# Kernel tuning notes

Hardware: AMD Instinct MI355X
Metric: run time of the kernel (lower is better)

## Reference

```python
import jax, jax.numpy as jnp
import numpy as np

EPS = 1e-5
L1, L2 = 1e-3, 1e-3
HEADS, HEAD_DIM = 8, 16


def ln(x):
    # torch.nn.LayerNorm over last dim, affine params at init (gamma=1, beta=0)
    m = jnp.mean(x, axis=-1, keepdims=True)
    v = jnp.var(x, axis=-1, keepdims=True)
    return (x - m) / jnp.sqrt(v + EPS)


def setup_inputs() -> dict:
    key = jax.random.key(0)
    ks = jax.random.split(key, 10)
    B, N, Dn = 16, 1000, 64
    D = HEADS * HEAD_DIM  # 128
    return {
        "nodevec_fusion": jax.random.normal(ks[0], (B, N, Dn), jnp.float32),
        "nodevec_s": jax.random.normal(ks[1], (N, Dn), jnp.float32),
        "node_input": jax.random.normal(ks[2], (B, N, Dn), jnp.float32),
        "nodevec_dy": jax.random.normal(ks[3], (N, Dn), jnp.float32),
        "w_q": jax.random.normal(ks[4], (Dn, D), jnp.float32) * 0.1,
        "w_k": jax.random.normal(ks[5], (Dn, D), jnp.float32) * 0.1,
        "node_w": jax.random.normal(ks[6], (N, Dn), jnp.float32) * 0.1,
        "mlp_w": jax.random.normal(ks[7], (HEADS, HEADS), jnp.float32) * 0.1,
        "mlp_b": jnp.zeros((HEADS,), jnp.float32),
        "attn_linear": jax.random.normal(ks[8], (N, N), jnp.float32) * 0.03,
        "attn_linear_1": jax.random.normal(ks[9], (N, N), jnp.float32) * 0.03,
        "batch_size": 16,
    }


def reference(nodevec_fusion, nodevec_s, node_input, nodevec_dy,
              w_q, w_k, node_w, mlp_w, mlp_b, attn_linear, attn_linear_1,
              batch_size):
    B = batch_size
    N, Dn = nodevec_s.shape
    H, hd = HEADS, HEAD_DIM

    # static graph: softmax(relu(LN(S S^T)), axis=1)
    s = nodevec_s @ nodevec_s.T                     # [N,N]
    adj_static = jax.nn.softmax(jax.nn.relu(ln(s)), axis=1)

    fusion = ln(nodevec_fusion)                     # [B,N,Dn]
    static_graph_inf = ln(nodevec_dy @ nodevec_dy.T)  # [N,N]

    # einsum('bnd,nl->bnl'): d is summed out of x only
    nv11 = jnp.einsum('bnd,nl->bnl', fusion, node_w) + fusion  # [B,N,Dn]
    skip_atten = ln(jnp.einsum('bnd,bmd->bnm', nv11, nv11))    # [B,N,N]

    # query/key fc layers (leaky_relu(x @ W)), then split D -> (H, hd)
    q = jax.nn.leaky_relu(jnp.einsum('bnd,do->bno', fusion, w_q))  # [B,N,D]
    k = jax.nn.leaky_relu(jnp.einsum('bnd,do->bno', fusion, w_k))  # [B,N,D]
    q = q.transpose(0, 2, 1).reshape(B, H, hd, N).transpose(0, 1, 3, 2)  # [B,H,N,hd]
    k = k.transpose(0, 2, 1).reshape(B, H, hd, N)                        # [B,H,hd,N]

    attention = jnp.einsum('bhnd,bhdm->bhnm', q, k) / (hd ** 0.5)  # [B,H,N,N]
    # 1x1 conv mixing heads + residual (dropout = 0)
    attention = jnp.einsum('oh,bhnm->bonm', mlp_w, attention) \
        + mlp_b[None, :, None, None] + attention

    adj_bf = ln(jnp.sum(attention, axis=1)) + skip_atten           # [B,N,N]
    adj_af = jax.nn.relu(jnp.einsum('bnm,ml->bnl', ln(adj_bf), attn_linear))
    adj_af = jnp.einsum('bnm,ml->bnl', adj_af, attn_linear_1)
    dy_adj_inf = ln(adj_af + adj_bf)
    dy_adj = ln(dy_adj_inf + static_graph_inf[None])
    adj_dynamic = jax.nn.softmax(jax.nn.relu(dy_adj), axis=2)

    adj_static_b = jnp.broadcast_to(adj_static[None], (B, N, N))

    # graph loss: sum_ij ||x_i - x_j||^2 * A_ij via squared-distance matmul trick
    sq = jnp.sum(node_input * node_input, axis=-1)                 # [B,N]
    gram = jnp.einsum('bnd,bmd->bnm', node_input, node_input)      # [B,N,N]
    d2 = sq[:, :, None] + sq[:, None, :] - 2.0 * gram              # [B,N,N]
    dist_loss = jnp.sum(d2 * adj_static_b, axis=(1, 2))            # [B]
    f_norm = jnp.sum(adj_static_b * adj_static_b, axis=(1, 2))     # [B]
    gl_loss = dist_loss * L1 + f_norm * L2

    return adj_dynamic, adj_static_b, nodevec_s, gl_loss
```

## Files before the change

### kernel.cpp

```cpp
#include <hip/hip_runtime.h>

#define B_  16
#define N_  1000
#define NP  1024
#define DN  64
#define D_  128

typedef __attribute__((ext_vector_type(8))) short  short8;
typedef __attribute__((ext_vector_type(4))) float  f32x4;
typedef __attribute__((ext_vector_type(4))) unsigned short ushort4v;

__device__ __forceinline__ unsigned short f2bf(float v) {
  union { float f; unsigned int u; } c; c.f = v;
  unsigned int u = c.u;
  unsigned int r = (u + 0x7fffu + ((u >> 16) & 1u)) >> 16;
  return (unsigned short)r;
}
__device__ __forceinline__ float bf2f(unsigned short h) {
  union { unsigned int u; float f; } c; c.u = ((unsigned int)h) << 16; return c.f;
}

__device__ __forceinline__ void block_red2(float& a, float& b) {
  __shared__ float sb[8];
  __syncthreads();
  float ra = a, rb = b;
  #pragma unroll
  for (int o = 32; o > 0; o >>= 1) { ra += __shfl_down(ra, o); rb += __shfl_down(rb, o); }
  int w = threadIdx.x >> 6;
  if ((threadIdx.x & 63) == 0) { sb[w] = ra; sb[4 + w] = rb; }
  __syncthreads();
  a = sb[0] + sb[1] + sb[2] + sb[3];
  b = sb[4] + sb[5] + sb[6] + sb[7];
}

__device__ __forceinline__ void block_redmax(float& a) {
  __shared__ float sm[4];
  __syncthreads();
  float ra = a;
  #pragma unroll
  for (int o = 32; o > 0; o >>= 1) ra = fmaxf(ra, __shfl_down(ra, o));
  if ((threadIdx.x & 63) == 0) sm[threadIdx.x >> 6] = ra;
  __syncthreads();
  a = fmaxf(fmaxf(sm[0], sm[1]), fmaxf(sm[2], sm[3]));
}

__global__ void prep_kernel(const float* __restrict__ mlp_w, const float* __restrict__ mlp_b,
                            const float* __restrict__ w_q, const float* __restrict__ w_k,
                            float* __restrict__ weff, float* __restrict__ tr,
                            float* __restrict__ fnorm, float* __restrict__ colsum,
                            unsigned short* __restrict__ wt) {
  int t = threadIdx.x;
  if (t < 8) {
    float s = 1.f;
    for (int o = 0; o < 8; ++o) s += mlp_w[o * 8 + t];
    weff[t] = s;
  }
  if (t < 16) tr[t] = 0.f;
  if (t == 16) fnorm[0] = 0.f;
  colsum[t] = 0.f;
  for (int i = t; i < 256 * 64; i += 1024) {
    int col = i >> 6, d = i & 63;
    float v = (col < 128) ? w_q[d * D_ + col] : w_k[d * D_ + (col - 128)];
    wt[i] = f2bf(v);
  }
  (void)mlp_b;
}

__global__ void transpose_pad(const float* __restrict__ in, unsigned short* __restrict__ out) {
  __shared__ float tile[32][33];
  int bx = blockIdx.x * 32, by = blockIdx.y * 32;
  int tx = threadIdx.x, ty = threadIdx.y;
  #pragma unroll
  for (int i = 0; i < 32; i += 8) {
    int r = by + ty + i, c = bx + tx;
    tile[ty + i][tx] = (r < N_ && c < N_) ? in[(long)r * N_ + c] : 0.f;
  }
  __syncthreads();
  #pragma unroll
  for (int i = 0; i < 32; i += 8) {
    int r = bx + ty + i, c = by + tx;
    out[(long)r * NP + c] = f2bf(tile[tx][ty + i]);
  }
}

__global__ void gram_kernel(const float* __restrict__ X, float* __restrict__ C, int ldc) {
  __shared__ float Xi[16][65], Xj[16][65];
  int tx = threadIdx.x, ty = threadIdx.y;
  int i0 = blockIdx.y * 16, j0 = blockIdx.x * 16;
  #pragma unroll
  for (int kk = 0; kk < 64; kk += 16) {
    int r = i0 + ty;  Xi[ty][kk + tx] = (r < N_) ? X[(long)r * DN + kk + tx] : 0.f;
    int rj = j0 + ty; Xj[ty][kk + tx] = (rj < N_) ? X[(long)rj * DN + kk + tx] : 0.f;
  }
  __syncthreads();
  float acc = 0.f;
  #pragma unroll
  for (int d = 0; d < 64; ++d) acc += Xi[ty][d] * Xj[tx][d];
  int i = i0 + ty, j = j0 + tx;
  if (i < N_ && j < N_) C[(long)i * ldc + j] = acc;
}

__global__ void row_ln(float* __restrict__ base, int ld) {
  int tid = threadIdx.x;
  float* row = base + (long)blockIdx.x * ld;
  float x[4]; float s = 0.f, s2 = 0.f;
  #pragma unroll
  for (int i = 0; i < 4; ++i) {
    int idx = tid + i * 256;
    x[i] = (idx < N_) ? row[idx] : 0.f;
    s += x[i]; s2 += x[i] * x[i];
  }
  block_red2(s, s2);
  float mean = s * 1e-3f, var = s2 * 1e-3f - mean * mean;
  float r = rsqrtf(var + 1e-5f);
  #pragma unroll
  for (int i = 0; i < 4; ++i) {
    int idx = tid + i * 256;
    if (idx < N_) row[idx] = (x[i] - mean) * r;
  }
}

__global__ void row_ln_sm(float* __restrict__ mat, float* __restrict__ rowsum) {
  int n = blockIdx.x, tid = threadIdx.x;
  float* row = mat + (long)n * N_;
  float x[4]; float s = 0.f, s2 = 0.f;
  #pragma unroll
  for (int i = 0; i < 4; ++i) {
    int idx = tid + i * 256;
    x[i] = (idx < N_) ? row[idx] : 0.f;
    s += x[i]; s2 += x[i] * x[i];
  }
  block_red2(s, s2);
  float mean = s * 1e-3f, var = s2 * 1e-3f - mean * mean;
  float r = rsqrtf(var + 1e-5f);
  float mx = -1e30f;
  #pragma unroll
  for (int i = 0; i < 4; ++i) {
    int idx = tid + i * 256;
    if (idx < N_) { x[i] = fmaxf((x[i] - mean) * r, 0.f); mx = fmaxf(mx, x[i]); }
  }
  block_redmax(mx);
  float es = 0.f, d = 0.f;
  #pragma unroll
  for (int i = 0; i < 4; ++i) {
    int idx = tid + i * 256;
    if (idx < N_) { x[i] = __expf(x[i] - mx); es += x[i]; } else x[i] = 0.f;
  }
  block_red2(es, d);
  float inv = 1.f / es; float ps = 0.f;
  #pragma unroll
  for (int i = 0; i < 4; ++i) {
    int idx = tid + i * 256;
    if (idx < N_) { x[i] *= inv; row[idx] = x[i]; ps += x[i]; }
  }
  d = 0.f; block_red2(ps, d);
  if (tid == 0) rowsum[n] = ps;
}

__global__ __launch_bounds__(256)
void fusion_ln(const float* __restrict__ fus, const float* __restrict__ node_w,
               const float* __restrict__ node_input,
               unsigned short* __restrict__ fbf, unsigned short* __restrict__ nv11,
               float* __restrict__ sq) {
  int wid = blockIdx.x * 4 + (threadIdx.x >> 6);
  int lane = threadIdx.x & 63;
  #pragma unroll 1
  for (int r = 0; r < 16; ++r) {
    int row = wid * 16 + r;
    int b = row >> 10, n = row & 1023;
    long po = (long)row * DN + lane;
    if (n < N_) {
      long io = ((long)b * N_ + n) * DN + lane;
      float xv = fus[io];
      float s = xv, s2 = xv * xv;
      #pragma unroll
      for (int o = 32; o > 0; o >>= 1) { s += __shfl_xor(s, o); s2 += __shfl_xor(s2, o); }
      float mean = s * (1.f / DN);
      float var  = s2 * (1.f / DN) - mean * mean;
      float fv = (xv - mean) * rsqrtf(var + 1e-5f);
      float rs = fv;
      #pragma unroll
      for (int o = 32; o > 0; o >>= 1) rs += __shfl_xor(rs, o);
      fbf[po]  = f2bf(fv);
      nv11[po] = f2bf(rs * node_w[(long)n * DN + lane] + fv);
      float xi = node_input[io];
      float q2 = xi * xi;
      #pragma unroll
      for (int o = 32; o > 0; o >>= 1) q2 += __shfl_xor(q2, o);
      if (lane == 0) sq[(long)b * N_ + n] = q2;
    } else {
      fbf[po] = 0; nv11[po] = 0;
    }
  }
}

#define GLOAD_LDS16(gp, lp) \
  __builtin_amdgcn_global_load_lds((const __attribute__((address_space(1))) void*)(gp), \
                                   (__attribute__((address_space(3))) void*)(lp), 16, 0, 0)

template<int EPI>
__global__ __launch_bounds__(256, 2)
void gemm_bt(const unsigned short* __restrict__ X, long xbs, int ldx,
             const unsigned short* __restrict__ Y, long ybs, int ldy,
             int K,
             unsigned short* __restrict__ outB, long obsB,
             const float* __restrict__ weff) {
  __shared__ __align__(16) short As[128 * 32];
  __shared__ __align__(16) short Bs[128 * 32];
  const int tid = threadIdx.x;
  const int b  = blockIdx.z;
  const int m0 = blockIdx.x * 128;
  const int n0 = blockIdx.y * 128;
  const unsigned short* Xb = X + (long)b * xbs + (long)m0 * ldx;
  const unsigned short* Yb = Y + (long)b * ybs + (long)n0 * ldy;

  const int lane = tid & 63, w = tid >> 6;
  const int wm = (w >> 1) * 64, wn = (w & 1) * 64;
  const int fr = lane & 15, kg = lane >> 4;

  const int sr = tid >> 2;
  const int ks = tid & 3;
  const int c1 = ((ks ^ ((sr >> 1) & 3)) * 8);
  const int c2 = ((ks ^ (((sr + 64) >> 1) & 3)) * 8);

  f32x4 acc[4][4];
  #pragma unroll
  for (int mi = 0; mi < 4; ++mi)
    #pragma unroll
    for (int ni = 0; ni < 4; ++ni)
      acc[mi][ni] = (f32x4){0.f, 0.f, 0.f, 0.f};

  const short* Asp = (const short*)As;
  const short* Bsp = (const short*)Bs;

  for (int k0 = 0; k0 < K; k0 += 32) {
    GLOAD_LDS16(Xb + (long)sr * ldx + k0 + c1,        (char*)As + tid * 16);
    GLOAD_LDS16(Xb + (long)(sr + 64) * ldx + k0 + c2, (char*)As + 4096 + tid * 16);
    GLOAD_LDS16(Yb + (long)sr * ldy + k0 + c1,        (char*)Bs + tid * 16);
    GLOAD_LDS16(Yb + (long)(sr + 64) * ldy + k0 + c2, (char*)Bs + 4096 + tid * 16);
    __syncthreads();
    short8 av[4], bv[4];
    #pragma unroll
    for (int mi = 0; mi < 4; ++mi) {
      int r = wm + mi * 16 + fr;
      av[mi] = *(const short8*)&Asp[r * 32 + ((kg ^ ((r >> 1) & 3)) * 8)];
    }
    #pragma unroll
    for (int ni = 0; ni < 4; ++ni) {
      int r = wn + ni * 16 + fr;
      bv[ni] = *(const short8*)&Bsp[r * 32 + ((kg ^ ((r >> 1) & 3)) * 8)];
    }
    #pragma unroll
    for (int mi = 0; mi < 4; ++mi)
      #pragma unroll
      for (int ni = 0; ni < 4; ++ni)
        acc[mi][ni] = __builtin_amdgcn_mfma_f32_16x16x32_bf16(av[mi], bv[ni], acc[mi][ni], 0, 0, 0);
    __syncthreads();
  }

  if (EPI == 1) {
    unsigned short* ob = outB + (long)b * obsB;
    #pragma unroll
    for (int mi = 0; mi < 4; ++mi) {
      #pragma unroll
      for (int ni = 0; ni < 4; ++ni) {
        int col  = n0 + wn + ni * 16 + fr;
        int rowb = m0 + wm + mi * 16 + kg * 4;
        #pragma unroll
        for (int j = 0; j < 4; ++j)
          ob[(long)(rowb + j) * NP + col] = f2bf(fmaxf(acc[mi][ni][j], 0.f));
      }
    }
  } else if (EPI == 2) {
    unsigned short* ob = outB;
    #pragma unroll
    for (int mi = 0; mi < 4; ++mi) {
      #pragma unroll
      for (int ni = 0; ni < 4; ++ni) {
        int col  = n0 + wn + ni * 16 + fr;
        int rowb = m0 + wm + mi * 16 + kg * 4;
        float sc = (col < 128) ? weff[col >> 4] * 0.25f : 1.f;
        #pragma unroll
        for (int j = 0; j < 4; ++j) {
          float v = acc[mi][ni][j];
          v = (v > 0.f) ? v : 0.01f * v;
          ob[(long)(rowb + j) * 256 + col] = f2bf(v * sc);
        }
      }
    }
  } else {
    unsigned short* ob = outB + (long)b * obsB;
    #pragma unroll
    for (int mi = 0; mi < 4; ++mi) {
      #pragma unroll
      for (int ni = 0; ni < 4; ++ni) {
        int col  = n0 + wn + ni * 16 + fr;
        int rowb = m0 + wm + mi * 16 + kg * 4;
        #pragma unroll
        for (int j = 0; j < 4; ++j)
          ob[(long)(rowb + j) * NP + col] = f2bf(acc[mi][ni][j]);
      }
    }
  }
}

__global__ __launch_bounds__(256)
void row_combine1(const unsigned short* __restrict__ apre, const unsigned short* __restrict__ skip,
                  unsigned short* __restrict__ adjbf, unsigned short* __restrict__ tbf) {
  int n = blockIdx.x, b = blockIdx.y, tid = threadIdx.x;
  long ro = ((long)b * NP + n) * NP + tid * 4;
  ushort4v a4 = *(const ushort4v*)(apre + ro);
  ushort4v s4 = *(const ushort4v*)(skip + ro);
  float xa[4], xs[4];
  float sa = 0.f, sa2 = 0.f, ss = 0.f, ss2 = 0.f;
  #pragma unroll
  for (int j = 0; j < 4; ++j) {
    bool mm = (tid * 4 + j) < N_;
    xa[j] = mm ? bf2f(a4[j]) : 0.f;
    xs[j] = mm ? bf2f(s4[j]) : 0.f;
    sa += xa[j]; sa2 += xa[j] * xa[j];
    ss += xs[j]; ss2 += xs[j] * xs[j];
  }
  block_red2(sa, sa2);
  block_red2(ss, ss2);
  float ma = sa * 1e-3f, ra = rsqrtf(sa2 * 1e-3f - ma * ma + 1e-5f);
  float ms = ss * 1e-3f, rs = rsqrtf(ss2 * 1e-3f - ms * ms + 1e-5f);
  float y[4]; float sy = 0.f, sy2 = 0.f;
  #pragma unroll
  for (int j = 0; j < 4; ++j) {
    y[j] = ((tid * 4 + j) < N_) ? (xa[j] - ma) * ra + (xs[j] - ms) * rs : 0.f;
    sy += y[j]; sy2 += y[j] * y[j];
  }
  block_red2(sy, sy2);
  float my = sy * 1e-3f, ry = rsqrtf(sy2 * 1e-3f - my * my + 1e-5f);
  ushort4v o1, o2;
  #pragma unroll
  for (int j = 0; j < 4; ++j) {
    o1[j] = f2bf(y[j]);
    o2[j] = ((tid * 4 + j) < N_) ? f2bf((y[j] - my) * ry) : (unsigned short)0;
  }
  *(ushort4v*)(adjbf + ro) = o1;
  *(ushort4v*)(tbf + ro) = o2;
}

__global__ __launch_bounds__(256)
void row_final(const unsigned short* __restrict__ g2, const unsigned short* __restrict__ adjbf,
               const float* __restrict__ sgi, float* __restrict__ outp) {
  int n = blockIdx.x, b = blockIdx.y, tid = threadIdx.x;
  long ro = ((long)b * NP + n) * NP + tid * 4;
  ushort4v g4 = *(const ushort4v*)(g2 + ro);
  ushort4v a4 = *(const ushort4v*)(adjbf + ro);
  float4 gr = *(const float4*)(sgi + (long)n * NP + tid * 4);
  const float* grp = (const float*)&gr;
  float x[4]; float s = 0.f, s2 = 0.f;
  #pragma unroll
  for (int j = 0; j < 4; ++j) {
    x[j] = ((tid * 4 + j) < N_) ? bf2f(g4[j]) + bf2f(a4[j]) : 0.f;
    s += x[j]; s2 += x[j] * x[j];
  }
  block_red2(s, s2);
  float m1 = s * 1e-3f, r1 = rsqrtf(s2 * 1e-3f - m1 * m1 + 1e-5f);
  s = 0.f; s2 = 0.f;
  #pragma unroll
  for (int j = 0; j < 4; ++j) {
    x[j] = ((tid * 4 + j) < N_) ? (x[j] - m1) * r1 + grp[j] : 0.f;
    s += x[j]; s2 += x[j] * x[j];
  }
  block_red2(s, s2);
  float m2 = s * 1e-3f, r2 = rsqrtf(s2 * 1e-3f - m2 * m2 + 1e-5f);
  float mx = -1e30f;
  #pragma unroll
  for (int j = 0; j < 4; ++j) {
    if ((tid * 4 + j) < N_) { x[j] = fmaxf((x[j] - m2) * r2, 0.f); mx = fmaxf(mx, x[j]); }
  }
  block_redmax(mx);
  float es = 0.f, dd = 0.f;
  #pragma unroll
  for (int j = 0; j < 4; ++j) {
    if ((tid * 4 + j) < N_) { x[j] = __expf(x[j] - mx); es += x[j]; } else x[j] = 0.f;
  }
  block_red2(es, dd);
  float inv = 1.f / es;
  if (tid < 250) {
    float4 o = make_float4(x[0] * inv, x[1] * inv, x[2] * inv, x[3] * inv);
    *(float4*)(outp + (long)b * 1000000 + (long)n * N_ + tid * 4) = o;
  }
}

__global__ void broadcast_static(const float* __restrict__ adjs, float* __restrict__ out1) {
  long i = (long)blockIdx.x * 256 + threadIdx.x;
  if (i < 250000) {
    float4 v = ((const float4*)adjs)[i];
    #pragma unroll
    for (int b = 0; b < B_; ++b) ((float4*)out1)[(long)b * 250000 + i] = v;
  }
}

__global__ void copy_s(const float* __restrict__ src, float* __restrict__ dst) {
  int i = blockIdx.x * 256 + threadIdx.x;
  if (i < N_ * DN) dst[i] = src[i];
}

__global__ void colsum_fnorm(const float* __restrict__ adjs, float* __restrict__ colsum,
                             float* __restrict__ fnorm) {
  int m = blockIdx.x * 256 + threadIdx.x;
  int n0 = blockIdx.y * 63;
  int ne = min(n0 + 63, N_);
  float c = 0.f, f = 0.f;
  if (m < N_) {
    for (int n = n0; n < ne; ++n) { float v = adjs[(long)n * N_ + m]; c += v; f += v * v; }
    atomicAdd(&colsum[m], c);
  }
  float d = 0.f; block_red2(f, d);
  if (threadIdx.x == 0) atomicAdd(fnorm, f);
}

__global__ __launch_bounds__(256)
void trace_kernel(const float* __restrict__ adjs, const float* __restrict__ x,
                  float* __restrict__ tr) {
  __shared__ float A_s[64 * 64];
  __shared__ float X_s[64 * 64];
  const int tid = threadIdx.x;
  const int tx = tid & 15, ty = tid >> 4;
  const int m0 = blockIdx.x * 64;
  const int b  = blockIdx.y;
  const int nseg = blockIdx.z;
  const float* xb = x + (long)b * (N_ * DN);

  float acc[4][4];
  #pragma unroll
  for (int i = 0; i < 4; ++i)
    #pragma unroll
    for (int j = 0; j < 4; ++j) acc[i][j] = 0.f;

  for (int cc = 0; cc < 4; ++cc) {
    int n0 = (nseg * 4 + cc) * 64;
    #pragma unroll
    for (int k = 0; k < 16; ++k) {
      int i = tid + k * 256;
      int nn = i >> 6, cm = i & 63;
      int n = n0 + nn;
      A_s[i] = (n < N_ && (m0 + cm) < N_) ? adjs[(long)n * N_ + m0 + cm] : 0.f;
      X_s[i] = (n < N_) ? xb[(long)n * DN + cm] : 0.f;
    }
    __syncthreads();
    #pragma unroll 8
    for (int nn = 0; nn < 64; ++nn) {
      float4 av = *(const float4*)&A_s[nn * 64 + ty * 4];
      float4 xv = *(const float4*)&X_s[nn * 64 + tx * 4];
      #pragma unroll
      for (int i = 0; i < 4; ++i) {
        float a = (&av.x)[i];
        acc[i][0] += a * xv.x;
        acc[i][1] += a * xv.y;
        acc[i][2] += a * xv.z;
        acc[i][3] += a * xv.w;
      }
    }
    __syncthreads();
  }

  float v = 0.f;
  #pragma unroll
  for (int i = 0; i < 4; ++i) {
    int m = m0 + ty * 4 + i;
    if (m < N_) {
      float4 xm = *(const float4*)&xb[(long)m * DN + tx * 4];
      v += acc[i][0] * xm.x + acc[i][1] * xm.y + acc[i][2] * xm.z + acc[i][3] * xm.w;
    }
  }
  float d = 0.f; block_red2(v, d);
  if (tid == 0) atomicAdd(&tr[b], v);
}

__global__ void gl_final(const float* __restrict__ sq, const float* __restrict__ rowsum,
                         const float* __restrict__ colsum, const float* __restrict__ tr,
                         const float* __restrict__ fnorm, float* __restrict__ gl) {
  int b = blockIdx.x, tid = threadIdx.x;
  float s = 0.f;
  for (int i = tid; i < N_; i += 256) s += sq[(long)b * N_ + i] * (rowsum[i] + colsum[i]);
  float d = 0.f; block_red2(s, d);
  if (tid == 0) gl[b] = (s - 2.f * tr[b]) * 1e-3f + fnorm[0] * 1e-3f;
}

extern "C" void kernel_launch(void* const* d_in, const int* in_sizes, int n_in,
                              void* d_out, int out_size, void* d_ws, size_t ws_size,
                              hipStream_t stream) {
  (void)in_sizes; (void)n_in; (void)out_size; (void)ws_size;
  const float* nodevec_fusion = (const float*)d_in[0];
  const float* nodevec_s      = (const float*)d_in[1];
  const float* node_input     = (const float*)d_in[2];
  const float* nodevec_dy     = (const float*)d_in[3];
  const float* w_q            = (const float*)d_in[4];
  const float* w_k            = (const float*)d_in[5];
  const float* node_w         = (const float*)d_in[6];
  const float* mlp_w          = (const float*)d_in[7];
  const float* mlp_b          = (const float*)d_in[8];
  const float* attn_linear    = (const float*)d_in[9];
  const float* attn_linear_1  = (const float*)d_in[10];

  float* out  = (float*)d_out;
  float* out0 = out;
  float* out1 = out + 16000000;
  float* outS = out + 32000000;
  float* outGL = out + 32064000;

  char* wp = (char*)d_ws;
  auto alloc = [&](size_t bytes) { char* p = wp; wp += (bytes + 255) & ~(size_t)255; return p; };
  float* adjs            = (float*)alloc((size_t)N_ * N_ * 4);
  float* sgi             = (float*)alloc((size_t)NP * NP * 4);
  unsigned short* apre   = (unsigned short*)alloc((size_t)B_ * NP * NP * 2);
  unsigned short* skipb  = (unsigned short*)alloc((size_t)B_ * NP * NP * 2);
  unsigned short* adjbf  = (unsigned short*)alloc((size_t)B_ * NP * NP * 2);
  unsigned short* tbf    = (unsigned short*)alloc((size_t)B_ * NP * NP * 2);
  unsigned short* afbf   = (unsigned short*)alloc((size_t)B_ * NP * NP * 2);
  unsigned short* L1T    = (unsigned short*)alloc((size_t)NP * NP * 2);
  unsigned short* L2T    = (unsigned short*)alloc((size_t)NP * NP * 2);
  unsigned short* nv11   = (unsigned short*)alloc((size_t)B_ * NP * DN * 2);
  unsigned short* fbf    = (unsigned short*)alloc((size_t)B_ * NP * DN * 2);
  unsigned short* qk     = (unsigned short*)alloc((size_t)B_ * NP * 256 * 2);
  unsigned short* wt     = (unsigned short*)alloc((size_t)256 * DN * 2);
  float* sq              = (float*)alloc((size_t)B_ * N_ * 4);
  float* colsum          = (float*)alloc(4096);
  float* rowsum          = (float*)alloc(4096);
  float* weff            = (float*)alloc(256);
  float* tr              = (float*)alloc(256);
  float* fnorm           = (float*)alloc(256);

  prep_kernel<<<1, 1024, 0, stream>>>(mlp_w, mlp_b, w_q, w_k, weff, tr, fnorm, colsum, wt);
  transpose_pad<<<dim3(32, 32), dim3(32, 8), 0, stream>>>(attn_linear,   L1T);
  transpose_pad<<<dim3(32, 32), dim3(32, 8), 0, stream>>>(attn_linear_1, L2T);
  gram_kernel<<<dim3(63, 63), dim3(16, 16), 0, stream>>>(nodevec_s,  adjs, N_);
  gram_kernel<<<dim3(63, 63), dim3(16, 16), 0, stream>>>(nodevec_dy, sgi, NP);
  row_ln_sm<<<1000, 256, 0, stream>>>(adjs, rowsum);
  row_ln<<<1000, 256, 0, stream>>>(sgi, NP);
  fusion_ln<<<256, 256, 0, stream>>>(nodevec_fusion, node_w, node_input, fbf, nv11, sq);
  gemm_bt<2><<<dim3(128, 2, 1), 256, 0, stream>>>(fbf, 0L, DN,
                                                  wt, 0L, DN, DN,
                                                  qk, 0L, weff);
  gemm_bt<3><<<dim3(8, 8, 16), 256, 0, stream>>>(nv11, (long)NP * DN, DN,
                                                 nv11, (long)NP * DN, DN, DN,
                                                 skipb, (long)NP * NP, (const float*)nullptr);
  gemm_bt<3><<<dim3(8, 8, 16), 256, 0, stream>>>(qk, (long)NP * 256, 256,
                                                 qk + 128, (long)NP * 256, 256, D_,
                                                 apre, (long)NP * NP, (const float*)nullptr);
  row_combine1<<<dim3(1000, 16), 256, 0, stream>>>(apre, skipb, adjbf, tbf);
  gemm_bt<1><<<dim3(8, 8, 16), 256, 0, stream>>>(tbf, (long)NP * NP, NP,
                                                 L1T, 0L, NP, NP,
                                                 afbf, (long)NP * NP, (const float*)nullptr);
  gemm_bt<3><<<dim3(8, 8, 16), 256, 0, stream>>>(afbf, (long)NP * NP, NP,
                                                 L2T, 0L, NP, NP,
                                                 apre, (long)NP * NP, (const float*)nullptr);
  row_final<<<dim3(1000, 16), 256, 0, stream>>>(apre, adjbf, sgi, out0);
  broadcast_static<<<977, 256, 0, stream>>>(adjs, out1);
  copy_s<<<250, 256, 0, stream>>>(nodevec_s, outS);
  colsum_fnorm<<<dim3(4, 16), 256, 0, stream>>>(adjs, colsum, fnorm);
  trace_kernel<<<dim3(16, 16, 4), 256, 0, stream>>>(adjs, node_input, tr);
  gl_final<<<16, 256, 0, stream>>>(sq, rowsum, colsum, tr, fnorm, outGL);
}
```

Baseline: 487.3 us.

## Use wave-per-row reductions, drop adjbf buffer via stats, retile gram kernel

The row-wise LayerNorm/softmax kernels now assign one 64-lane wavefront per row and reduce with xor shuffles, which removes the block-level shared-memory reductions and barriers. row_combine1 no longer writes the adj_bf tensor. It stores a per-row mean and std instead, and row_final rebuilds adj_bf from the normalized tbf, saving one bf16 B×N×N write and read. The gram kernel moves to 64x64 tiles with 4x4 register blocking and float4 stores. The rebuilt adj_bf carries an extra bf16 rounding step, which may change numerics slightly.

```diff
diff --git a/kernel.cpp b/kernel.cpp
--- a/kernel.cpp
+++ b/kernel.cpp
@@ -8,7 +8,7 @@
 
 typedef __attribute__((ext_vector_type(8))) short  short8;
 typedef __attribute__((ext_vector_type(4))) float  f32x4;
-typedef __attribute__((ext_vector_type(4))) unsigned short ushort4v;
+typedef __attribute__((ext_vector_type(8))) unsigned short ushort8v;
 
 __device__ __forceinline__ unsigned short f2bf(float v) {
   union { float f; unsigned int u; } c; c.f = v;
@@ -18,6 +18,17 @@
 }
 __device__ __forceinline__ float bf2f(unsigned short h) {
   union { unsigned int u; float f; } c; c.u = ((unsigned int)h) << 16; return c.f;
+}
+
+__device__ __forceinline__ float wred(float v) {
+  #pragma unroll
+  for (int o = 32; o > 0; o >>= 1) v += __shfl_xor(v, o);
+  return v;
+}
+__device__ __forceinline__ float wredmax(float v) {
+  #pragma unroll
+  for (int o = 32; o > 0; o >>= 1) v = fmaxf(v, __shfl_xor(v, o));
+  return v;
 }
 
 __device__ __forceinline__ void block_red2(float& a, float& b) {
@@ -31,17 +42,6 @@
   __syncthreads();
   a = sb[0] + sb[1] + sb[2] + sb[3];
   b = sb[4] + sb[5] + sb[6] + sb[7];
-}
-
-__device__ __forceinline__ void block_redmax(float& a) {
-  __shared__ float sm[4];
-  __syncthreads();
-  float ra = a;
-  #pragma unroll
-  for (int o = 32; o > 0; o >>= 1) ra = fmaxf(ra, __shfl_down(ra, o));
-  if ((threadIdx.x & 63) == 0) sm[threadIdx.x >> 6] = ra;
-  __syncthreads();
-  a = fmaxf(fmaxf(sm[0], sm[1]), fmaxf(sm[2], sm[3]));
 }
 
 __global__ void prep_kernel(const float* __restrict__ mlp_w, const float* __restrict__ mlp_b,
@@ -83,78 +83,143 @@
   }
 }
 
-__global__ void gram_kernel(const float* __restrict__ X, float* __restrict__ C, int ldc) {
-  __shared__ float Xi[16][65], Xj[16][65];
-  int tx = threadIdx.x, ty = threadIdx.y;
-  int i0 = blockIdx.y * 16, j0 = blockIdx.x * 16;
-  #pragma unroll
-  for (int kk = 0; kk < 64; kk += 16) {
-    int r = i0 + ty;  Xi[ty][kk + tx] = (r < N_) ? X[(long)r * DN + kk + tx] : 0.f;
-    int rj = j0 + ty; Xj[ty][kk + tx] = (rj < N_) ? X[(long)rj * DN + kk + tx] : 0.f;
+__global__ __launch_bounds__(256)
+void gram_kernel(const float* __restrict__ X, float* __restrict__ C, int ldc) {
+  __shared__ float Xi[64 * 67];
+  __shared__ float Xj[64 * 67];
+  const int tid = threadIdx.x;
+  const int tx = tid & 15, ty = tid >> 4;
+  const int i0 = blockIdx.y * 64, j0 = blockIdx.x * 64;
+  #pragma unroll
+  for (int t = 0; t < 16; ++t) {
+    int e = tid + t * 256;
+    int r = e >> 6, c = e & 63;
+    int ri = i0 + r, rj = j0 + r;
+    Xi[r * 67 + c] = (ri < N_) ? X[(long)ri * DN + c] : 0.f;
+    Xj[r * 67 + c] = (rj < N_) ? X[(long)rj * DN + c] : 0.f;
   }
   __syncthreads();
-  float acc = 0.f;
-  #pragma unroll
-  for (int d = 0; d < 64; ++d) acc += Xi[ty][d] * Xj[tx][d];
-  int i = i0 + ty, j = j0 + tx;
-  if (i < N_ && j < N_) C[(long)i * ldc + j] = acc;
-}
-
-__global__ void row_ln(float* __restrict__ base, int ld) {
-  int tid = threadIdx.x;
-  float* row = base + (long)blockIdx.x * ld;
-  float x[4]; float s = 0.f, s2 = 0.f;
+  float acc[4][4];
+  #pragma unroll
+  for (int i = 0; i < 4; ++i)
+    #pragma unroll
+    for (int j = 0; j < 4; ++j) acc[i][j] = 0.f;
+  #pragma unroll 4
+  for (int d = 0; d < 64; ++d) {
+    float av[4], bv[4];
+    #pragma unroll
+    for (int i = 0; i < 4; ++i) av[i] = Xi[(ty * 4 + i) * 67 + d];
+    #pragma unroll
+    for (int j = 0; j < 4; ++j) bv[j] = Xj[(tx * 4 + j) * 67 + d];
+    #pragma unroll
+    for (int i = 0; i < 4; ++i)
+      #pragma unroll
+      for (int j = 0; j < 4; ++j) acc[i][j] += av[i] * bv[j];
+  }
+  int cc = j0 + tx * 4;
   #pragma unroll
   for (int i = 0; i < 4; ++i) {
-    int idx = tid + i * 256;
-    x[i] = (idx < N_) ? row[idx] : 0.f;
-    s += x[i]; s2 += x[i] * x[i];
-  }
-  block_red2(s, s2);
-  float mean = s * 1e-3f, var = s2 * 1e-3f - mean * mean;
-  float r = rsqrtf(var + 1e-5f);
-  #pragma unroll
-  for (int i = 0; i < 4; ++i) {
-    int idx = tid + i * 256;
-    if (idx < N_) row[idx] = (x[i] - mean) * r;
-  }
-}
-
-__global__ void row_ln_sm(float* __restrict__ mat, float* __restrict__ rowsum) {
-  int n = blockIdx.x, tid = threadIdx.x;
+    int r = i0 + ty * 4 + i;
+    if (r < N_ && cc < N_) {
+      float4 o = make_float4(acc[i][0], acc[i][1], acc[i][2], acc[i][3]);
+      *(float4*)&C[(long)r * ldc + cc] = o;
+    }
+  }
+}
+
+__global__ __launch_bounds__(256)
+void row_ln(float* __restrict__ base, int ld) {
+  int w = threadIdx.x >> 6, lane = threadIdx.x & 63;
+  int n = blockIdx.x * 4 + w;
+  float* row = base + (long)n * ld;
+  float x[16]; float s = 0.f, s2 = 0.f;
+  #pragma unroll
+  for (int c = 0; c < 2; ++c) {
+    int bse = c * 512 + lane * 8;
+    if (bse < N_) {
+      float4 v0 = *(const float4*)(row + bse);
+      float4 v1 = *(const float4*)(row + bse + 4);
+      x[c*8+0]=v0.x; x[c*8+1]=v0.y; x[c*8+2]=v0.z; x[c*8+3]=v0.w;
+      x[c*8+4]=v1.x; x[c*8+5]=v1.y; x[c*8+6]=v1.z; x[c*8+7]=v1.w;
+    } else {
+      #pragma unroll
+      for (int j = 0; j < 8; ++j) x[c*8+j] = 0.f;
+    }
+    #pragma unroll
+    for (int j = 0; j < 8; ++j) { s += x[c*8+j]; s2 += x[c*8+j]*x[c*8+j]; }
+  }
+  s = wred(s); s2 = wred(s2);
+  float mean = s * 1e-3f, r = rsqrtf(s2 * 1e-3f - mean * mean + 1e-5f);
+  #pragma unroll
+  for (int c = 0; c < 2; ++c) {
+    int bse = c * 512 + lane * 8;
+    if (bse < N_) {
+      float4 o0 = make_float4((x[c*8+0]-mean)*r, (x[c*8+1]-mean)*r, (x[c*8+2]-mean)*r, (x[c*8+3]-mean)*r);
+      float4 o1 = make_float4((x[c*8+4]-mean)*r, (x[c*8+5]-mean)*r, (x[c*8+6]-mean)*r, (x[c*8+7]-mean)*r);
+      *(float4*)(row + bse) = o0;
+      *(float4*)(row + bse + 4) = o1;
+    }
+  }
+}
+
+__global__ __launch_bounds__(256)
+void row_ln_sm(float* __restrict__ mat, float* __restrict__ rowsum) {
+  int w = threadIdx.x >> 6, lane = threadIdx.x & 63;
+  int n = blockIdx.x * 4 + w;
   float* row = mat + (long)n * N_;
-  float x[4]; float s = 0.f, s2 = 0.f;
-  #pragma unroll
-  for (int i = 0; i < 4; ++i) {
-    int idx = tid + i * 256;
-    x[i] = (idx < N_) ? row[idx] : 0.f;
-    s += x[i]; s2 += x[i] * x[i];
-  }
-  block_red2(s, s2);
-  float mean = s * 1e-3f, var = s2 * 1e-3f - mean * mean;
-  float r = rsqrtf(var + 1e-5f);
+  float x[16]; float s = 0.f, s2 = 0.f;
+  #pragma unroll
+  for (int c = 0; c < 2; ++c) {
+    int bse = c * 512 + lane * 8;
+    if (bse < N_) {
+      float4 v0 = *(const float4*)(row + bse);
+      float4 v1 = *(const float4*)(row + bse + 4);
+      x[c*8+0]=v0.x; x[c*8+1]=v0.y; x[c*8+2]=v0.z; x[c*8+3]=v0.w;
+      x[c*8+4]=v1.x; x[c*8+5]=v1.y; x[c*8+6]=v1.z; x[c*8+7]=v1.w;
+    } else {
+      #pragma unroll
+      for (int j = 0; j < 8; ++j) x[c*8+j] = 0.f;
+    }
+    #pragma unroll
+    for (int j = 0; j < 8; ++j) { s += x[c*8+j]; s2 += x[c*8+j]*x[c*8+j]; }
+  }
+  s = wred(s); s2 = wred(s2);
+  float mean = s * 1e-3f, r = rsqrtf(s2 * 1e-3f - mean * mean + 1e-5f);
   float mx = -1e30f;
   #pragma unroll
-  for (int i = 0; i < 4; ++i) {
-    int idx = tid + i * 256;
-    if (idx < N_) { x[i] = fmaxf((x[i] - mean) * r, 0.f); mx = fmaxf(mx, x[i]); }
-  }
-  block_redmax(mx);
-  float es = 0.f, d = 0.f;
-  #pragma unroll
-  for (int i = 0; i < 4; ++i) {
-    int idx = tid + i * 256;
-    if (idx < N_) { x[i] = __expf(x[i] - mx); es += x[i]; } else x[i] = 0.f;
-  }
-  block_red2(es, d);
+  for (int c = 0; c < 2; ++c) {
+    int bse = c * 512 + lane * 8;
+    #pragma unroll
+    for (int j = 0; j < 8; ++j) {
+      if (bse < N_) { x[c*8+j] = fmaxf((x[c*8+j]-mean)*r, 0.f); mx = fmaxf(mx, x[c*8+j]); }
+    }
+  }
+  mx = wredmax(mx);
+  float es = 0.f;
+  #pragma unroll
+  for (int c = 0; c < 2; ++c) {
+    int bse = c * 512 + lane * 8;
+    #pragma unroll
+    for (int j = 0; j < 8; ++j) {
+      if (bse < N_) { x[c*8+j] = __expf(x[c*8+j] - mx); es += x[c*8+j]; } else x[c*8+j] = 0.f;
+    }
+  }
+  es = wred(es);
   float inv = 1.f / es; float ps = 0.f;
   #pragma unroll
-  for (int i = 0; i < 4; ++i) {
-    int idx = tid + i * 256;
-    if (idx < N_) { x[i] *= inv; row[idx] = x[i]; ps += x[i]; }
-  }
-  d = 0.f; block_red2(ps, d);
-  if (tid == 0) rowsum[n] = ps;
+  for (int c = 0; c < 2; ++c) {
+    int bse = c * 512 + lane * 8;
+    #pragma unroll
+    for (int j = 0; j < 8; ++j) { x[c*8+j] *= inv; ps += x[c*8+j]; }
+    if (bse < N_) {
+      float4 o0 = make_float4(x[c*8+0], x[c*8+1], x[c*8+2], x[c*8+3]);
+      float4 o1 = make_float4(x[c*8+4], x[c*8+5], x[c*8+6], x[c*8+7]);
+      *(float4*)(row + bse) = o0;
+      *(float4*)(row + bse + 4) = o1;
+    }
+  }
+  ps = wred(ps);
+  if (lane == 0) rowsum[n] = ps;
 }
 
 __global__ __launch_bounds__(256)
@@ -306,84 +371,127 @@
 
 __global__ __launch_bounds__(256)
 void row_combine1(const unsigned short* __restrict__ apre, const unsigned short* __restrict__ skip,
-                  unsigned short* __restrict__ adjbf, unsigned short* __restrict__ tbf) {
-  int n = blockIdx.x, b = blockIdx.y, tid = threadIdx.x;
-  long ro = ((long)b * NP + n) * NP + tid * 4;
-  ushort4v a4 = *(const ushort4v*)(apre + ro);
-  ushort4v s4 = *(const ushort4v*)(skip + ro);
-  float xa[4], xs[4];
+                  unsigned short* __restrict__ tbf, float2* __restrict__ stat) {
+  int w = threadIdx.x >> 6, lane = threadIdx.x & 63;
+  int n = blockIdx.x * 4 + w, b = blockIdx.y;
+  long base = ((long)b * NP + n) * NP;
+  ushort8v a8[2], s8[2];
+  #pragma unroll
+  for (int c = 0; c < 2; ++c) {
+    a8[c] = *(const ushort8v*)(apre + base + c * 512 + lane * 8);
+    s8[c] = *(const ushort8v*)(skip + base + c * 512 + lane * 8);
+  }
+  float xa[16], xs[16];
   float sa = 0.f, sa2 = 0.f, ss = 0.f, ss2 = 0.f;
   #pragma unroll
-  for (int j = 0; j < 4; ++j) {
-    bool mm = (tid * 4 + j) < N_;
-    xa[j] = mm ? bf2f(a4[j]) : 0.f;
-    xs[j] = mm ? bf2f(s4[j]) : 0.f;
-    sa += xa[j]; sa2 += xa[j] * xa[j];
-    ss += xs[j]; ss2 += xs[j] * xs[j];
-  }
-  block_red2(sa, sa2);
-  block_red2(ss, ss2);
+  for (int c = 0; c < 2; ++c)
+    #pragma unroll
+    for (int j = 0; j < 8; ++j) {
+      bool mm = (c * 512 + lane * 8 + j) < N_;
+      float va = mm ? bf2f(a8[c][j]) : 0.f;
+      float vs = mm ? bf2f(s8[c][j]) : 0.f;
+      xa[c*8+j] = va; xs[c*8+j] = vs;
+      sa += va; sa2 += va * va; ss += vs; ss2 += vs * vs;
+    }
+  sa = wred(sa); sa2 = wred(sa2); ss = wred(ss); ss2 = wred(ss2);
   float ma = sa * 1e-3f, ra = rsqrtf(sa2 * 1e-3f - ma * ma + 1e-5f);
   float ms = ss * 1e-3f, rs = rsqrtf(ss2 * 1e-3f - ms * ms + 1e-5f);
-  float y[4]; float sy = 0.f, sy2 = 0.f;
-  #pragma unroll
-  for (int j = 0; j < 4; ++j) {
-    y[j] = ((tid * 4 + j) < N_) ? (xa[j] - ma) * ra + (xs[j] - ms) * rs : 0.f;
-    sy += y[j]; sy2 += y[j] * y[j];
-  }
-  block_red2(sy, sy2);
-  float my = sy * 1e-3f, ry = rsqrtf(sy2 * 1e-3f - my * my + 1e-5f);
-  ushort4v o1, o2;
-  #pragma unroll
-  for (int j = 0; j < 4; ++j) {
-    o1[j] = f2bf(y[j]);
-    o2[j] = ((tid * 4 + j) < N_) ? f2bf((y[j] - my) * ry) : (unsigned short)0;
-  }
-  *(ushort4v*)(adjbf + ro) = o1;
-  *(ushort4v*)(tbf + ro) = o2;
+  float y[16]; float sy = 0.f, sy2 = 0.f;
+  #pragma unroll
+  for (int c = 0; c < 2; ++c)
+    #pragma unroll
+    for (int j = 0; j < 8; ++j) {
+      bool mm = (c * 512 + lane * 8 + j) < N_;
+      y[c*8+j] = mm ? (xa[c*8+j] - ma) * ra + (xs[c*8+j] - ms) * rs : 0.f;
+      sy += y[c*8+j]; sy2 += y[c*8+j] * y[c*8+j];
+    }
+  sy = wred(sy); sy2 = wred(sy2);
+  float my = sy * 1e-3f, vy = sy2 * 1e-3f - my * my;
+  float ry = rsqrtf(vy + 1e-5f);
+  #pragma unroll
+  for (int c = 0; c < 2; ++c) {
+    ushort8v o;
+    #pragma unroll
+    for (int j = 0; j < 8; ++j) {
+      bool mm = (c * 512 + lane * 8 + j) < N_;
+      o[j] = mm ? f2bf((y[c*8+j] - my) * ry) : (unsigned short)0;
+    }
+    *(ushort8v*)(tbf + base + c * 512 + lane * 8) = o;
+  }
+  if (lane == 0) stat[(long)b * NP + n] = make_float2(my, sqrtf(vy + 1e-5f));
 }
 
 __global__ __launch_bounds__(256)
-void row_final(const unsigned short* __restrict__ g2, const unsigned short* __restrict__ adjbf,
-               const float* __restrict__ sgi, float* __restrict__ outp) {
-  int n = blockIdx.x, b = blockIdx.y, tid = threadIdx.x;
-  long ro = ((long)b * NP + n) * NP + tid * 4;
-  ushort4v g4 = *(const ushort4v*)(g2 + ro);
-  ushort4v a4 = *(const ushort4v*)(adjbf + ro);
-  float4 gr = *(const float4*)(sgi + (long)n * NP + tid * 4);
-  const float* grp = (const float*)&gr;
-  float x[4]; float s = 0.f, s2 = 0.f;
-  #pragma unroll
-  for (int j = 0; j < 4; ++j) {
-    x[j] = ((tid * 4 + j) < N_) ? bf2f(g4[j]) + bf2f(a4[j]) : 0.f;
-    s += x[j]; s2 += x[j] * x[j];
-  }
-  block_red2(s, s2);
+void row_final(const unsigned short* __restrict__ g2, const unsigned short* __restrict__ tbf,
+               const float2* __restrict__ stat, const float* __restrict__ sgi,
+               float* __restrict__ outp) {
+  int w = threadIdx.x >> 6, lane = threadIdx.x & 63;
+  int n = blockIdx.x * 4 + w, b = blockIdx.y;
+  long base = ((long)b * NP + n) * NP;
+  float2 st = stat[(long)b * NP + n];
+  ushort8v g8[2], t8[2];
+  float gr[16];
+  #pragma unroll
+  for (int c = 0; c < 2; ++c) {
+    g8[c] = *(const ushort8v*)(g2  + base + c * 512 + lane * 8);
+    t8[c] = *(const ushort8v*)(tbf + base + c * 512 + lane * 8);
+    float4 v0 = *(const float4*)(sgi + (long)n * NP + c * 512 + lane * 8);
+    float4 v1 = *(const float4*)(sgi + (long)n * NP + c * 512 + lane * 8 + 4);
+    gr[c*8+0]=v0.x; gr[c*8+1]=v0.y; gr[c*8+2]=v0.z; gr[c*8+3]=v0.w;
+    gr[c*8+4]=v1.x; gr[c*8+5]=v1.y; gr[c*8+6]=v1.z; gr[c*8+7]=v1.w;
+  }
+  float x[16]; float s = 0.f, s2 = 0.f;
+  #pragma unroll
+  for (int c = 0; c < 2; ++c)
+    #pragma unroll
+    for (int j = 0; j < 8; ++j) {
+      bool mm = (c * 512 + lane * 8 + j) < N_;
+      x[c*8+j] = mm ? bf2f(g8[c][j]) + (bf2f(t8[c][j]) * st.y + st.x) : 0.f;
+      s += x[c*8+j]; s2 += x[c*8+j] * x[c*8+j];
+    }
+  s = wred(s); s2 = wred(s2);
   float m1 = s * 1e-3f, r1 = rsqrtf(s2 * 1e-3f - m1 * m1 + 1e-5f);
   s = 0.f; s2 = 0.f;
   #pragma unroll
-  for (int j = 0; j < 4; ++j) {
-    x[j] = ((tid * 4 + j) < N_) ? (x[j] - m1) * r1 + grp[j] : 0.f;
-    s += x[j]; s2 += x[j] * x[j];
-  }
-  block_red2(s, s2);
+  for (int c = 0; c < 2; ++c)
+    #pragma unroll
+    for (int j = 0; j < 8; ++j) {
+      bool mm = (c * 512 + lane * 8 + j) < N_;
+      x[c*8+j] = mm ? (x[c*8+j] - m1) * r1 + gr[c*8+j] : 0.f;
+      s += x[c*8+j]; s2 += x[c*8+j] * x[c*8+j];
+    }
+  s = wred(s); s2 = wred(s2);
   float m2 = s * 1e-3f, r2 = rsqrtf(s2 * 1e-3f - m2 * m2 + 1e-5f);
   float mx = -1e30f;
   #pragma unroll
-  for (int j = 0; j < 4; ++j) {
-    if ((tid * 4 + j) < N_) { x[j] = fmaxf((x[j] - m2) * r2, 0.f); mx = fmaxf(mx, x[j]); }
-  }
-  block_redmax(mx);
-  float es = 0.f, dd = 0.f;
-  #pragma unroll
-  for (int j = 0; j < 4; ++j) {
-    if ((tid * 4 + j) < N_) { x[j] = __expf(x[j] - mx); es += x[j]; } else x[j] = 0.f;
-  }
-  block_red2(es, dd);
+  for (int c = 0; c < 2; ++c)
+    #pragma unroll
+    for (int j = 0; j < 8; ++j) {
+      if ((c * 512 + lane * 8 + j) < N_) {
+        x[c*8+j] = fmaxf((x[c*8+j] - m2) * r2, 0.f); mx = fmaxf(mx, x[c*8+j]);
+      }
+    }
+  mx = wredmax(mx);
+  float es = 0.f;
+  #pragma unroll
+  for (int c = 0; c < 2; ++c)
+    #pragma unroll
+    for (int j = 0; j < 8; ++j) {
+      if ((c * 512 + lane * 8 + j) < N_) { x[c*8+j] = __expf(x[c*8+j] - mx); es += x[c*8+j]; }
+      else x[c*8+j] = 0.f;
+    }
+  es = wred(es);
   float inv = 1.f / es;
-  if (tid < 250) {
-    float4 o = make_float4(x[0] * inv, x[1] * inv, x[2] * inv, x[3] * inv);
-    *(float4*)(outp + (long)b * 1000000 + (long)n * N_ + tid * 4) = o;
+  float* orow = outp + (long)b * 1000000 + (long)n * N_;
+  #pragma unroll
+  for (int c = 0; c < 2; ++c) {
+    int bse = c * 512 + lane * 8;
+    if (bse < N_) {
+      float4 o0 = make_float4(x[c*8+0]*inv, x[c*8+1]*inv, x[c*8+2]*inv, x[c*8+3]*inv);
+      float4 o1 = make_float4(x[c*8+4]*inv, x[c*8+5]*inv, x[c*8+6]*inv, x[c*8+7]*inv);
+      *(float4*)(orow + bse) = o0;
+      *(float4*)(orow + bse + 4) = o1;
+    }
   }
 }
 
@@ -511,7 +619,6 @@
   float* sgi             = (float*)alloc((size_t)NP * NP * 4);
   unsigned short* apre   = (unsigned short*)alloc((size_t)B_ * NP * NP * 2);
   unsigned short* skipb  = (unsigned short*)alloc((size_t)B_ * NP * NP * 2);
-  unsigned short* adjbf  = (unsigned short*)alloc((size_t)B_ * NP * NP * 2);
   unsigned short* tbf    = (unsigned short*)alloc((size_t)B_ * NP * NP * 2);
   unsigned short* afbf   = (unsigned short*)alloc((size_t)B_ * NP * NP * 2);
   unsigned short* L1T    = (unsigned short*)alloc((size_t)NP * NP * 2);
@@ -520,6 +627,7 @@
   unsigned short* fbf    = (unsigned short*)alloc((size_t)B_ * NP * DN * 2);
   unsigned short* qk     = (unsigned short*)alloc((size_t)B_ * NP * 256 * 2);
   unsigned short* wt     = (unsigned short*)alloc((size_t)256 * DN * 2);
+  float2* stat           = (float2*)alloc((size_t)B_ * NP * 8);
   float* sq              = (float*)alloc((size_t)B_ * N_ * 4);
   float* colsum          = (float*)alloc(4096);
   float* rowsum          = (float*)alloc(4096);
@@ -530,10 +638,10 @@
   prep_kernel<<<1, 1024, 0, stream>>>(mlp_w, mlp_b, w_q, w_k, weff, tr, fnorm, colsum, wt);
   transpose_pad<<<dim3(32, 32), dim3(32, 8), 0, stream>>>(attn_linear,   L1T);
   transpose_pad<<<dim3(32, 32), dim3(32, 8), 0, stream>>>(attn_linear_1, L2T);
-  gram_kernel<<<dim3(63, 63), dim3(16, 16), 0, stream>>>(nodevec_s,  adjs, N_);
-  gram_kernel<<<dim3(63, 63), dim3(16, 16), 0, stream>>>(nodevec_dy, sgi, NP);
-  row_ln_sm<<<1000, 256, 0, stream>>>(adjs, rowsum);
-  row_ln<<<1000, 256, 0, stream>>>(sgi, NP);
+  gram_kernel<<<dim3(16, 16), 256, 0, stream>>>(nodevec_s,  adjs, N_);
+  gram_kernel<<<dim3(16, 16), 256, 0, stream>>>(nodevec_dy, sgi, NP);
+  row_ln_sm<<<250, 256, 0, stream>>>(adjs, rowsum);
+  row_ln<<<250, 256, 0, stream>>>(sgi, NP);
   fusion_ln<<<256, 256, 0, stream>>>(nodevec_fusion, node_w, node_input, fbf, nv11, sq);
   gemm_bt<2><<<dim3(128, 2, 1), 256, 0, stream>>>(fbf, 0L, DN,
                                                   wt, 0L, DN, DN,
@@ -544,14 +652,14 @@
   gemm_bt<3><<<dim3(8, 8, 16), 256, 0, stream>>>(qk, (long)NP * 256, 256,
                                                  qk + 128, (long)NP * 256, 256, D_,
                                                  apre, (long)NP * NP, (const float*)nullptr);
-  row_combine1<<<dim3(1000, 16), 256, 0, stream>>>(apre, skipb, adjbf, tbf);
+  row_combine1<<<dim3(250, 16), 256, 0, stream>>>(apre, skipb, tbf, stat);
   gemm_bt<1><<<dim3(8, 8, 16), 256, 0, stream>>>(tbf, (long)NP * NP, NP,
                                                  L1T, 0L, NP, NP,
                                                  afbf, (long)NP * NP, (const float*)nullptr);
   gemm_bt<3><<<dim3(8, 8, 16), 256, 0, stream>>>(afbf, (long)NP * NP, NP,
                                                  L2T, 0L, NP, NP,
                                                  apre, (long)NP * NP, (const float*)nullptr);
-  row_final<<<dim3(1000, 16), 256, 0, stream>>>(apre, adjbf, sgi, out0);
+  row_final<<<dim3(250, 16), 256, 0, stream>>>(apre, tbf, stat, sgi, out0);
   broadcast_static<<<977, 256, 0, stream>>>(adjs, out1);
   copy_s<<<250, 256, 0, stream>>>(nodevec_s, outS);
   colsum_fnorm<<<dim3(4, 16), 256, 0, stream>>>(adjs, colsum, fnorm);
```

After: 471.8 us. -3.2%, faster.
